# Kernel optimization log

Hardware: AMD Instinct MI355X
Metric: run time of the kernel (lower is better)

The kernel has to match this reference:

```python
import jax, jax.numpy as jnp
import numpy as np

B, L, D, FF = 4, 4096, 1024, 2048
EPS = 1e-5


def _ln(x, g, b):
    m = jnp.mean(x, axis=-1, keepdims=True)
    v = jnp.var(x, axis=-1, keepdims=True)
    return (x - m) / jnp.sqrt(v + EPS) * g + b


def setup_inputs() -> dict:
    key = jax.random.key(0)
    ks = jax.random.split(key, 9)
    x = jax.random.normal(ks[0], (B, L, D), jnp.float32)
    # phazor init: exp(2j*pi*k/D) * |randn| -> split into re/im float params
    mag = jnp.abs(jax.random.normal(ks[1], (D,), jnp.float32))
    ang = 2.0 * jnp.pi * jnp.arange(D, dtype=jnp.float32) / D
    return dict(
        x=x,
        ln_g=jnp.ones((D,), jnp.float32),
        ln_b=jnp.zeros((D,), jnp.float32),
        fc_w=jax.random.normal(ks[2], (D, D), jnp.float32) * 0.02,
        fc_b=jnp.zeros((D,), jnp.float32),
        w1=jax.random.normal(ks[3], (D, FF), jnp.float32) * 0.02,
        b1=jnp.zeros((FF,), jnp.float32),
        w2=jax.random.normal(ks[4], (FF, D), jnp.float32) * 0.02,
        b2=jnp.zeros((D,), jnp.float32),
        ph_re=mag * jnp.cos(ang),
        ph_im=mag * jnp.sin(ang),
        phi_re=jax.random.normal(ks[5], (D,), jnp.float32),
        phi_im=jax.random.normal(ks[6], (D,), jnp.float32),
        lci_re=jax.random.normal(ks[7], (D,), jnp.float32),
        lci_im=jax.random.normal(ks[8], (D,), jnp.float32),
    )


def _spiral_conv(xn, ph_re, ph_im, phi_re, phi_im, lci_re, lci_im):
    ph = ph_re + 1j * ph_im          # phazor parameter [D]
    phi = phi_re + 1j * phi_im       # phazor_init [D]
    lci = lci_re + 1j * lci_im       # last_conv_init [D]
    a = jnp.abs(ph)
    phz = ph / a * jnp.exp(-a)       # unit direction * decaying magnitude, [D]
    t = jnp.arange(L, dtype=jnp.float32)[:, None]
    prog = jnp.exp(t * jnp.log(phz)[None, :])        # phz**t, [L, D]
    filt = prog * phi[None, :]                       # [L, D]
    filt_fft = jnp.fft.fft(filt, n=2 * L, axis=0)    # [2L, D]
    x_fft = jnp.fft.fft(xn.astype(jnp.complex64), n=2 * L, axis=1)  # [B, 2L, D]
    conv = jnp.fft.ifft(filt_fft[None] * x_fft, axis=1)[:, :L]      # [B, L, D]
    # last_conv is detached in the original (first call uses last_conv_init)
    last = jax.lax.stop_gradient(lci)
    conv = conv + last[None, None, :] * prog[None] * phz[None, None, :]
    return conv.real


def reference(x, ln_g, ln_b, fc_w, fc_b, w1, b1, w2, b2,
              ph_re, ph_im, phi_re, phi_im, lci_re, lci_im):
    xn = _ln(x, ln_g, ln_b)
    c = _spiral_conv(xn, ph_re, ph_im, phi_re, phi_im, lci_re, lci_im)
    y = jax.nn.silu(x @ fc_w + fc_b)
    x2 = c * y + x                  # gated conv + residual (dropout=0 -> identity)
    x3 = _ln(x2, ln_g, ln_b)        # same (shared) LayerNorm instance
    h = jax.nn.silu(x3 @ w1 + b1) @ w2 + b2
    return x2 + h
```

## Files before the change

kernel.cpp:

```cpp
#include <hip/hip_runtime.h>
#include <hip/hip_bf16.h>
#include <hip/hip_fp8.h>
#include <cstdint>
#include <cstddef>

#define B_ 4
#define L_ 4096
#define D_ 1024
#define FF_ 2048
#define ROWS (B_ * L_)
#define EPS_ 1e-5f
#define CG 64
#define CC 64

typedef __attribute__((ext_vector_type(8))) __bf16 bf16x8;
typedef __attribute__((ext_vector_type(4))) float f32x4;
typedef __attribute__((ext_vector_type(4))) unsigned short us4;

__device__ __forceinline__ float bf2f(unsigned short u) {
  union { unsigned int i; float f; } v; v.i = ((unsigned int)u) << 16; return v.f;
}
__device__ __forceinline__ unsigned short f2bf(float f) {
  union { float f; unsigned int i; } v; v.f = f;
  unsigned int r = v.i + 0x7fffu + ((v.i >> 16) & 1u);
  return (unsigned short)(r >> 16);
}
__device__ __forceinline__ unsigned char f2fp8(float f) {
  __hip_fp8_e4m3 q(f);
  return *reinterpret_cast<unsigned char*>(&q);
}

__global__ __launch_bounds__(256) void transpose_cast(
    const float* __restrict__ in, unsigned short* __restrict__ out, int K, int N) {
  __shared__ float tb[32][33];
  int n0 = blockIdx.x * 32, k0 = blockIdx.y * 32;
  int tx = threadIdx.x & 31, ty = threadIdx.x >> 5;
#pragma unroll
  for (int i = 0; i < 4; ++i) {
    int k = ty + i * 8;
    tb[k][tx] = in[(size_t)(k0 + k) * N + n0 + tx];
  }
  __syncthreads();
#pragma unroll
  for (int i = 0; i < 4; ++i) {
    int n = ty + i * 8;
    out[(size_t)(n0 + n) * K + k0 + tx] = f2bf(tb[tx][n]);
  }
}

__global__ __launch_bounds__(256) void transpose_cast_fp8(
    const float* __restrict__ in, unsigned char* __restrict__ out, int K, int N,
    float scale) {
  __shared__ float tb[32][33];
  int n0 = blockIdx.x * 32, k0 = blockIdx.y * 32;
  int tx = threadIdx.x & 31, ty = threadIdx.x >> 5;
#pragma unroll
  for (int i = 0; i < 4; ++i) {
    int k = ty + i * 8;
    tb[k][tx] = in[(size_t)(k0 + k) * N + n0 + tx];
  }
  __syncthreads();
#pragma unroll
  for (int i = 0; i < 4; ++i) {
    int n = ty + i * 8;
    out[(size_t)(n0 + n) * K + k0 + tx] = f2fp8(tb[tx][n] * scale);
  }
}

__global__ __launch_bounds__(256) void ln1_kernel(
    const float* __restrict__ x, const float* __restrict__ g, const float* __restrict__ b,
    unsigned short* __restrict__ xn, unsigned short* __restrict__ xb) {
  int row = blockIdx.x;
  int t = threadIdx.x;
  const float4* xr = (const float4*)(x + (size_t)row * D_);
  float4 v = xr[t];
  float s = v.x + v.y + v.z + v.w;
  float sq = v.x * v.x + v.y * v.y + v.z * v.z + v.w * v.w;
#pragma unroll
  for (int off = 32; off > 0; off >>= 1) {
    s += __shfl_down(s, off);
    sq += __shfl_down(sq, off);
  }
  __shared__ float ls[4], lq[4];
  int lane = t & 63, w = t >> 6;
  if (lane == 0) { ls[w] = s; lq[w] = sq; }
  __syncthreads();
  s = ls[0] + ls[1] + ls[2] + ls[3];
  sq = lq[0] + lq[1] + lq[2] + lq[3];
  float mean = s * (1.0f / D_);
  float var = sq * (1.0f / D_) - mean * mean;
  float rstd = rsqrtf(var + EPS_);
  float4 gv = ((const float4*)g)[t];
  float4 bv = ((const float4*)b)[t];
  us4 o, ob;
  o.x = f2bf((v.x - mean) * rstd * gv.x + bv.x);
  o.y = f2bf((v.y - mean) * rstd * gv.y + bv.y);
  o.z = f2bf((v.z - mean) * rstd * gv.z + bv.z);
  o.w = f2bf((v.w - mean) * rstd * gv.w + bv.w);
  ob.x = f2bf(v.x); ob.y = f2bf(v.y); ob.z = f2bf(v.z); ob.w = f2bf(v.w);
  ((us4*)(xn + (size_t)row * D_))[t] = o;
  ((us4*)(xb + (size_t)row * D_))[t] = ob;
}

__global__ __launch_bounds__(256) void conv_pass1(
    const unsigned short* __restrict__ xn, const float* __restrict__ ph_re,
    const float* __restrict__ ph_im, float2* __restrict__ rloc) {
  int d = blockIdx.x * 256 + threadIdx.x;
  int g = blockIdx.y, b = blockIdx.z;
  float re = ph_re[d], im = ph_im[d];
  float a = sqrtf(re * re + im * im);
  float sc = expf(-a) / a;
  float pr = re * sc, pi = im * sc;
  float rr = 0.f, ri = 0.f;
  const unsigned short* xp = xn + ((size_t)(b * L_ + g * CC)) * D_ + d;
#pragma unroll 8
  for (int l = 0; l < CC; ++l) {
    float xv = bf2f(xp[(size_t)l * D_]);
    float nr = pr * rr - pi * ri + xv;
    ri = pr * ri + pi * rr;
    rr = nr;
  }
  rloc[((size_t)(b * CG + g)) * D_ + d] = make_float2(rr, ri);
}

__global__ __launch_bounds__(256) void conv_pass2(
    const float* __restrict__ ph_re, const float* __restrict__ ph_im,
    const float2* __restrict__ rloc, float2* __restrict__ carry) {
  int idx = blockIdx.x * 256 + threadIdx.x;
  int b = idx >> 10, d = idx & (D_ - 1);
  float re = ph_re[d], im = ph_im[d];
  float a = sqrtf(re * re + im * im);
  float th = atan2f(im, re);
  float rho = expf(-a * (float)CC);
  float ang = th * (float)CC;
  float pcr = rho * cosf(ang), pci = rho * sinf(ang);
  float cr = 0.f, ci = 0.f;
  for (int g0 = 0; g0 < CG; g0 += 8) {
    float2 rl[8];
    float2 cw[8];
#pragma unroll
    for (int i = 0; i < 8; ++i)
      rl[i] = rloc[((size_t)(b * CG + g0 + i)) * D_ + d];
#pragma unroll
    for (int i = 0; i < 8; ++i) {
      cw[i] = make_float2(cr, ci);
      float nr = pcr * cr - pci * ci + rl[i].x;
      ci = pcr * ci + pci * cr + rl[i].y;
      cr = nr;
    }
#pragma unroll
    for (int i = 0; i < 8; ++i)
      carry[((size_t)(b * CG + g0 + i)) * D_ + d] = cw[i];
  }
}

__global__ __launch_bounds__(256) void conv_pass3(
    const unsigned short* __restrict__ xn,
    const float* __restrict__ ph_re, const float* __restrict__ ph_im,
    const float* __restrict__ phi_re, const float* __restrict__ phi_im,
    const float* __restrict__ lci_re, const float* __restrict__ lci_im,
    const float2* __restrict__ carry, unsigned short* __restrict__ cout) {
  int d = blockIdx.x * 256 + threadIdx.x;
  int g = blockIdx.y, b = blockIdx.z;
  float re = ph_re[d], im = ph_im[d];
  float a = sqrtf(re * re + im * im);
  float sc = expf(-a) / a;
  float pr = re * sc, pi = im * sc;
  float th = atan2f(im, re);
  int l0 = g * CC;
  float rho = expf(-a * (float)(l0 + 1));
  float ang = th * (float)(l0 + 1);
  float prr = rho * cosf(ang), pri = rho * sinf(ang);
  float fr = phi_re[d], fi = phi_im[d];
  float qr = lci_re[d], qi = lci_im[d];
  float2 cv = carry[((size_t)(b * CG + g)) * D_ + d];
  float rr = cv.x, ri = cv.y;
  const unsigned short* xp = xn + ((size_t)(b * L_ + l0)) * D_ + d;
  unsigned short* cp = cout + ((size_t)(b * L_ + l0)) * D_ + d;
#pragma unroll 4
  for (int l = 0; l < CC; ++l) {
    float xv = bf2f(xp[(size_t)l * D_]);
    float nr = pr * rr - pi * ri + xv;
    ri = pr * ri + pi * rr;
    rr = nr;
    float outv = fr * rr - fi * ri + qr * prr - qi * pri;
    cp[(size_t)l * D_] = f2bf(outv);
    float pn = pr * prr - pi * pri;
    pri = pr * pri + pi * prr;
    prr = pn;
  }
}

__global__ __launch_bounds__(256) void ln2c_kernel(
    const unsigned short* __restrict__ x2, const float* __restrict__ g,
    const float* __restrict__ b, unsigned char* __restrict__ x3) {
  int row = blockIdx.x;
  int t = threadIdx.x;
  size_t base = (size_t)row * D_;
  us4 vb = ((const us4*)(x2 + base))[t];
  float4 v;
  v.x = bf2f(vb.x); v.y = bf2f(vb.y); v.z = bf2f(vb.z); v.w = bf2f(vb.w);
  float s = v.x + v.y + v.z + v.w;
  float sq = v.x * v.x + v.y * v.y + v.z * v.z + v.w * v.w;
#pragma unroll
  for (int off = 32; off > 0; off >>= 1) {
    s += __shfl_down(s, off);
    sq += __shfl_down(sq, off);
  }
  __shared__ float ls[4], lq[4];
  int lane = t & 63, w = t >> 6;
  if (lane == 0) { ls[w] = s; lq[w] = sq; }
  __syncthreads();
  s = ls[0] + ls[1] + ls[2] + ls[3];
  sq = lq[0] + lq[1] + lq[2] + lq[3];
  float mean = s * (1.0f / D_);
  float var = sq * (1.0f / D_) - mean * mean;
  float rstd = rsqrtf(var + EPS_);
  float4 gv = ((const float4*)g)[t];
  float4 bv = ((const float4*)b)[t];
  uchar4 o;
  o.x = f2fp8((v.x - mean) * rstd * gv.x + bv.x);
  o.y = f2fp8((v.y - mean) * rstd * gv.y + bv.y);
  o.z = f2fp8((v.z - mean) * rstd * gv.z + bv.z);
  o.w = f2fp8((v.w - mean) * rstd * gv.w + bv.w);
  ((uchar4*)(x3 + base))[t] = o;
}

__device__ __forceinline__ void gld_lds16(const void* gp, void* lp) {
  __builtin_amdgcn_global_load_lds(
      (const __attribute__((address_space(1))) unsigned int*)gp,
      (__attribute__((address_space(3))) unsigned int*)lp, 16, 0, 0);
}

#define PHASE_SYNC()                                         \
  __builtin_amdgcn_s_barrier();                              \
  asm volatile("s_waitcnt lgkmcnt(0)" ::: "memory");         \
  __builtin_amdgcn_sched_barrier(0);                         \
  __builtin_amdgcn_s_setprio(1);

#define PHASE_END()                                          \
  __builtin_amdgcn_s_setprio(0);

__global__ __launch_bounds__(512) void gemm_bt_gate(
    const unsigned short* __restrict__ A, const unsigned short* __restrict__ Bt,
    const float* __restrict__ bias,
    const unsigned short* __restrict__ gate, const float* __restrict__ xresf,
    unsigned short* __restrict__ Cv, int NB, int GROUP, int N, int K) {
  __shared__ unsigned short As[3][256 * 64];
  __shared__ unsigned short Bs[3][128 * 64];

  int nwg = gridDim.x;
  int xcd = blockIdx.x & 7;
  int lo = blockIdx.x >> 3;
  int q = nwg >> 3;
  int gsz = GROUP * NB;
  int g_ = lo / gsz, r_ = lo % gsz;
  int n_ = r_ / GROUP, ml = r_ - n_ * GROUP;
  int Mx = q / NB;
  int bm0 = (xcd * Mx + g_ * GROUP + ml) * 256;
  int bn0 = n_ * 128;

  int t = threadIdx.x;
  int lane = t & 63, w = t >> 6;
  int wr = w >> 1, wc = w & 1;
  int frr = lane & 15, cl = lane >> 4;
  int fx = frr & 7;
  int rA0 = wr * 64 + frr;
  int rB0 = wc * 64 + frr;
  int ko0 = (cl ^ fx) * 8;
  int ko1 = ((4 + cl) ^ fx) * 8;

  int nt = K >> 6;

  int tr = t >> 3;
  int jx = (t & 7) ^ (tr & 7);
  const unsigned short* pA = A + (size_t)(bm0 + tr) * K + jx * 8;
  const unsigned short* pB = Bt + (size_t)(bn0 + tr) * K + jx * 8;

  auto stA = [&](int kt2, int slot, int c) {
    gld_lds16(pA + (size_t)kt2 * 64 + (size_t)c * 64 * K, &As[slot][c * 4096 + t * 8]);
  };
  auto stB = [&](int kt2, int slot, int c) {
    gld_lds16(pB + (size_t)kt2 * 64 + (size_t)c * 64 * K, &Bs[slot][c * 4096 + t * 8]);
  };

  f32x4 acc[4][4] = {};

  stA(0, 0, 0); stA(0, 0, 1); stA(0, 0, 2); stA(0, 0, 3); stB(0, 0, 0); stB(0, 0, 1);
  stA(1, 1, 0); stA(1, 1, 1); stA(1, 1, 2); stA(1, 1, 3); stB(1, 1, 0); stB(1, 1, 1);
  asm volatile("s_waitcnt vmcnt(6)" ::: "memory");
  __builtin_amdgcn_s_barrier();

  int s = 0;
  for (int kt = 0; kt < nt; ++kt) {
    const unsigned short* as = As[s];
    const unsigned short* bs = Bs[s];
    int s2 = s + 2; if (s2 >= 3) s2 -= 3;
    bool p2 = kt + 2 < nt;

    bf16x8 a0[4], b0[4];
#pragma unroll
    for (int m = 0; m < 4; ++m) a0[m] = *(const bf16x8*)&as[(rA0 + m * 16) * 64 + ko0];
#pragma unroll
    for (int n = 0; n < 4; ++n) b0[n] = *(const bf16x8*)&bs[(rB0 + n * 16) * 64 + ko0];
    if (p2) { stA(kt + 2, s2, 0); stA(kt + 2, s2, 1); stB(kt + 2, s2, 0); }
    PHASE_SYNC();
#pragma unroll
    for (int m = 0; m < 4; ++m)
#pragma unroll
      for (int n = 0; n < 4; ++n)
        acc[m][n] = __builtin_amdgcn_mfma_f32_16x16x32_bf16(a0[m], b0[n], acc[m][n], 0, 0, 0);
    PHASE_END();
    __builtin_amdgcn_s_barrier();

    bf16x8 a1[4], b1[4];
#pragma unroll
    for (int m = 0; m < 4; ++m) a1[m] = *(const bf16x8*)&as[(rA0 + m * 16) * 64 + ko1];
#pragma unroll
    for (int n = 0; n < 4; ++n) b1[n] = *(const bf16x8*)&bs[(rB0 + n * 16) * 64 + ko1];
    if (p2) { stA(kt + 2, s2, 2); stA(kt + 2, s2, 3); stB(kt + 2, s2, 1); }
    PHASE_SYNC();
#pragma unroll
    for (int m = 0; m < 4; ++m)
#pragma unroll
      for (int n = 0; n < 4; ++n)
        acc[m][n] = __builtin_amdgcn_mfma_f32_16x16x32_bf16(a1[m], b1[n], acc[m][n], 0, 0, 0);
    PHASE_END();
    if (p2) { asm volatile("s_waitcnt vmcnt(6)" ::: "memory"); }
    else    { asm volatile("s_waitcnt vmcnt(0)" ::: "memory"); }
    __builtin_amdgcn_s_barrier();
    s += 1; if (s == 3) s = 0;
  }

#pragma unroll
  for (int m = 0; m < 4; ++m) {
#pragma unroll
    for (int n = 0; n < 4; ++n) {
#pragma unroll
      for (int r = 0; r < 4; ++r) {
        int row = bm0 + wr * 64 + m * 16 + cl * 4 + r;
        int col = bn0 + wc * 64 + n * 16 + frr;
        size_t o = (size_t)row * N + col;
        float v = acc[m][n][r] + bias[col];
        v = v / (1.0f + __expf(-v));
        v = bf2f(gate[o]) * v + xresf[o];
        Cv[o] = f2bf(v);
      }
    }
  }
}

template <int SILU, int RESBF, int OUT_FP8>
__global__ __launch_bounds__(512, 4) void gemm_f8(
    const unsigned char* __restrict__ A, const unsigned char* __restrict__ Bt,
    const float* __restrict__ bias, const unsigned short* __restrict__ resb,
    float oscale, void* __restrict__ Cv, int NB, int GROUP, int N, int K) {
  __shared__ unsigned char As[3][256 * 64];
  __shared__ unsigned char Bs[3][128 * 64];

  int nwg = gridDim.x;
  int xcd = blockIdx.x & 7;
  int lo = blockIdx.x >> 3;
  int q = nwg >> 3;
  int gsz = GROUP * NB;
  int g_ = lo / gsz, r_ = lo % gsz;
  int n_ = r_ / GROUP, ml = r_ - n_ * GROUP;
  int Mx = q / NB;
  int bm0 = (xcd * Mx + g_ * GROUP + ml) * 256;
  int bn0 = n_ * 128;

  int t = threadIdx.x;
  int lane = t & 63, w = t >> 6;
  int wr = w >> 1, wc = w & 1;
  int frr = lane & 15, cl = lane >> 4;
  int sw = (frr >> 1) & 3;
  int rA0 = wr * 64 + frr;
  int rB0 = wc * 64 + frr;
  int ko0 = ((((cl >> 1) ^ sw) << 4) | ((cl & 1) << 3));
  int ko1 = (((((cl >> 1) + 2) ^ sw) << 4) | ((cl & 1) << 3));

  int nt = K >> 6;

  int tr = t >> 2;
  int jc = (t & 3) ^ ((tr >> 1) & 3);
  const unsigned char* pA = A + (size_t)(bm0 + tr) * K + jc * 16;
  const unsigned char* pB = Bt + (size_t)(bn0 + tr) * K + jc * 16;

  auto stA = [&](int kt2, int slot, int c) {
    gld_lds16(pA + (size_t)kt2 * 64 + (size_t)c * 128 * K, &As[slot][c * 8192 + t * 16]);
  };
  auto stB = [&](int kt2, int slot) {
    gld_lds16(pB + (size_t)kt2 * 64, &Bs[slot][t * 16]);
  };

  f32x4 acc[4][4] = {};

  stA(0, 0, 0); stA(0, 0, 1); stB(0, 0);
  stA(1, 1, 0); stA(1, 1, 1); stB(1, 1);
  asm volatile("s_waitcnt vmcnt(3)" ::: "memory");
  __builtin_amdgcn_s_barrier();

  int s = 0;
  for (int kt = 0; kt < nt; ++kt) {
    const unsigned char* as = As[s];
    const unsigned char* bs = Bs[s];
    int s2 = s + 2; if (s2 >= 3) s2 -= 3;
    bool p2 = kt + 2 < nt;

    long a0[4], b0[4], a1[4], b1[4];
#pragma unroll
    for (int m = 0; m < 4; ++m) a0[m] = *(const long*)&as[(rA0 + m * 16) * 64 + ko0];
#pragma unroll
    for (int n = 0; n < 4; ++n) b0[n] = *(const long*)&bs[(rB0 + n * 16) * 64 + ko0];
#pragma unroll
    for (int m = 0; m < 4; ++m) a1[m] = *(const long*)&as[(rA0 + m * 16) * 64 + ko1];
#pragma unroll
    for (int n = 0; n < 4; ++n) b1[n] = *(const long*)&bs[(rB0 + n * 16) * 64 + ko1];
    if (p2) { stA(kt + 2, s2, 0); stA(kt + 2, s2, 1); stB(kt + 2, s2); }

    asm volatile("s_waitcnt lgkmcnt(0)" ::: "memory");
    __builtin_amdgcn_sched_barrier(0);
    __builtin_amdgcn_s_setprio(1);
#pragma unroll
    for (int m = 0; m < 4; ++m)
#pragma unroll
      for (int n = 0; n < 4; ++n)
        acc[m][n] = __builtin_amdgcn_mfma_f32_16x16x32_fp8_fp8(a0[m], b0[n], acc[m][n], 0, 0, 0);
#pragma unroll
    for (int m = 0; m < 4; ++m)
#pragma unroll
      for (int n = 0; n < 4; ++n)
        acc[m][n] = __builtin_amdgcn_mfma_f32_16x16x32_fp8_fp8(a1[m], b1[n], acc[m][n], 0, 0, 0);
    __builtin_amdgcn_s_setprio(0);

    if (p2) { asm volatile("s_waitcnt vmcnt(3)" ::: "memory"); }
    else    { asm volatile("s_waitcnt vmcnt(0)" ::: "memory"); }
    __builtin_amdgcn_s_barrier();
    s += 1; if (s == 3) s = 0;
  }

#pragma unroll
  for (int m = 0; m < 4; ++m) {
#pragma unroll
    for (int n = 0; n < 4; ++n) {
#pragma unroll
      for (int r = 0; r < 4; ++r) {
        int row = bm0 + wr * 64 + m * 16 + cl * 4 + r;
        int col = bn0 + wc * 64 + n * 16 + frr;
        size_t o = (size_t)row * N + col;
        float v = acc[m][n][r] * oscale + bias[col];
        if (SILU) v = v / (1.0f + __expf(-v));
        if (RESBF) v += bf2f(resb[o]);
        if (OUT_FP8)
          ((unsigned char*)Cv)[o] = f2fp8(v);
        else
          ((float*)Cv)[o] = v;
      }
    }
  }
}

extern "C" void kernel_launch(void* const* d_in, const int* in_sizes, int n_in,
                              void* d_out, int out_size, void* d_ws, size_t ws_size,
                              hipStream_t stream) {
  const float* x      = (const float*)d_in[0];
  const float* ln_g   = (const float*)d_in[1];
  const float* ln_b   = (const float*)d_in[2];
  const float* fc_w   = (const float*)d_in[3];
  const float* fc_b   = (const float*)d_in[4];
  const float* w1     = (const float*)d_in[5];
  const float* b1     = (const float*)d_in[6];
  const float* w2     = (const float*)d_in[7];
  const float* b2     = (const float*)d_in[8];
  const float* ph_re  = (const float*)d_in[9];
  const float* ph_im  = (const float*)d_in[10];
  const float* phi_re = (const float*)d_in[11];
  const float* phi_im = (const float*)d_in[12];
  const float* lci_re = (const float*)d_in[13];
  const float* lci_im = (const float*)d_in[14];
  float* out = (float*)d_out;

  char* ws = (char*)d_ws;
  const size_t SZ_BF = (size_t)ROWS * D_ * 2;
  const size_t SZ_F8 = (size_t)ROWS * D_;
  unsigned short* xn_x2 = (unsigned short*)(ws);
  unsigned short* cbuf  = (unsigned short*)(ws + SZ_BF);
  unsigned short* xb    = (unsigned short*)(ws + 2 * SZ_BF);
  unsigned char*  x3f8  = (unsigned char*)(ws + 3 * SZ_BF);
  unsigned char*  h1f8  = (unsigned char*)(ws + 3 * SZ_BF + SZ_F8);
  char* wp = ws + 3 * SZ_BF + SZ_F8 + (size_t)ROWS * FF_;
  unsigned short* fc_wt = (unsigned short*)(wp);
  unsigned char*  w1t8  = (unsigned char*)(wp + (size_t)D_ * D_ * 2);
  unsigned char*  w2t8  = (unsigned char*)(wp + (size_t)D_ * D_ * 2 + (size_t)D_ * FF_);
  float2* rloc  = (float2*)(wp + (size_t)D_ * D_ * 2 + 2 * (size_t)D_ * FF_);
  float2* carry = rloc + (size_t)B_ * CG * D_;

  transpose_cast<<<dim3(D_ / 32, D_ / 32), 256, 0, stream>>>(fc_w, fc_wt, D_, D_);
  transpose_cast_fp8<<<dim3(FF_ / 32, D_ / 32), 256, 0, stream>>>(w1, w1t8, D_, FF_, 32.0f);
  transpose_cast_fp8<<<dim3(D_ / 32, FF_ / 32), 256, 0, stream>>>(w2, w2t8, FF_, D_, 32.0f);

  ln1_kernel<<<ROWS, 256, 0, stream>>>(x, ln_g, ln_b, xn_x2, xb);

  conv_pass1<<<dim3(D_ / 256, CG, B_), 256, 0, stream>>>(xn_x2, ph_re, ph_im, rloc);
  conv_pass2<<<dim3((B_ * D_) / 256), 256, 0, stream>>>(ph_re, ph_im, rloc, carry);
  conv_pass3<<<dim3(D_ / 256, CG, B_), 256, 0, stream>>>(xn_x2, ph_re, ph_im, phi_re, phi_im,
                                                         lci_re, lci_im, carry, cbuf);

  gemm_bt_gate<<<(ROWS / 256) * (D_ / 128), 512, 0, stream>>>(
      xb, fc_wt, fc_b, cbuf, x, xn_x2, D_ / 128, 4, D_, D_);

  ln2c_kernel<<<ROWS, 256, 0, stream>>>(xn_x2, ln_g, ln_b, x3f8);

  gemm_f8<1, 0, 1><<<(ROWS / 256) * (FF_ / 128), 512, 0, stream>>>(
      x3f8, w1t8, b1, nullptr, 1.0f / 32.0f, h1f8, FF_ / 128, 4, FF_, D_);

  gemm_f8<0, 1, 0><<<(ROWS / 256) * (D_ / 128), 512, 0, stream>>>(
      h1f8, w2t8, b2, xn_x2, 1.0f / 32.0f, out, D_ / 128, 2, D_, FF_);
}
```

Baseline: 269.5 us.

## Permute FP8 operand layout for 128-bit LDS reads; single-phase bf16 gate GEMM loop

The FP8 operands (transposed weights, LN2 output, FF1 output) are now written in a permuted order within each 64-byte K chunk. This lets the FP8 GEMM fetch both k-halves with a single 16-byte LDS read per fragment instead of two 8-byte reads. Separately, the bf16 gate GEMM drops its two-phase barrier-split loop: it loads all fragments up front, issues all prefetches together, and runs both MFMA halves under one priority raise. The risk is that every producer and consumer must agree on the permutation, and the bf16 loop loses the intra-tile barrier overlap while holding more fragment registers live.

```diff
diff --git a/kernel.cpp b/kernel.cpp
--- a/kernel.cpp
+++ b/kernel.cpp
@@ -16,6 +16,7 @@
 typedef __attribute__((ext_vector_type(8))) __bf16 bf16x8;
 typedef __attribute__((ext_vector_type(4))) float f32x4;
 typedef __attribute__((ext_vector_type(4))) unsigned short us4;
+typedef __attribute__((ext_vector_type(2))) long l2;
 
 __device__ __forceinline__ float bf2f(unsigned short u) {
   union { unsigned int i; float f; } v; v.i = ((unsigned int)u) << 16; return v.f;
@@ -28,6 +29,9 @@
 __device__ __forceinline__ unsigned char f2fp8(float f) {
   __hip_fp8_e4m3 q(f);
   return *reinterpret_cast<unsigned char*>(&q);
+}
+__device__ __forceinline__ int ph64(int e) {
+  return (((e >> 3) & 3) << 4) | (((e >> 5) & 1) << 3) | (e & 7);
 }
 
 __global__ __launch_bounds__(256) void transpose_cast(
@@ -63,7 +67,9 @@
 #pragma unroll
   for (int i = 0; i < 4; ++i) {
     int n = ty + i * 8;
-    out[(size_t)(n0 + n) * K + k0 + tx] = f2fp8(tb[tx][n] * scale);
+    int k = k0 + tx;
+    size_t idx = (size_t)(n0 + n) * K + (k & ~63) + ph64(k & 63);
+    out[idx] = f2fp8(tb[tx][n] * scale);
   }
 }
 
@@ -223,7 +229,9 @@
   o.y = f2fp8((v.y - mean) * rstd * gv.y + bv.y);
   o.z = f2fp8((v.z - mean) * rstd * gv.z + bv.z);
   o.w = f2fp8((v.w - mean) * rstd * gv.w + bv.w);
-  ((uchar4*)(x3 + base))[t] = o;
+  int d = t * 4;
+  size_t idx = base + (size_t)((d & ~63) + ph64(d & 63));
+  *((uchar4*)(x3 + idx)) = o;
 }
 
 __device__ __forceinline__ void gld_lds16(const void* gp, void* lp) {
@@ -231,15 +239,6 @@
       (const __attribute__((address_space(1))) unsigned int*)gp,
       (__attribute__((address_space(3))) unsigned int*)lp, 16, 0, 0);
 }
-
-#define PHASE_SYNC()                                         \
-  __builtin_amdgcn_s_barrier();                              \
-  asm volatile("s_waitcnt lgkmcnt(0)" ::: "memory");         \
-  __builtin_amdgcn_sched_barrier(0);                         \
-  __builtin_amdgcn_s_setprio(1);
-
-#define PHASE_END()                                          \
-  __builtin_amdgcn_s_setprio(0);
 
 __global__ __launch_bounds__(512) void gemm_bt_gate(
     const unsigned short* __restrict__ A, const unsigned short* __restrict__ Bt,
@@ -298,34 +297,35 @@
     int s2 = s + 2; if (s2 >= 3) s2 -= 3;
     bool p2 = kt + 2 < nt;
 
-    bf16x8 a0[4], b0[4];
+    bf16x8 a0[4], b0[4], a1[4], b1[4];
 #pragma unroll
     for (int m = 0; m < 4; ++m) a0[m] = *(const bf16x8*)&as[(rA0 + m * 16) * 64 + ko0];
 #pragma unroll
     for (int n = 0; n < 4; ++n) b0[n] = *(const bf16x8*)&bs[(rB0 + n * 16) * 64 + ko0];
-    if (p2) { stA(kt + 2, s2, 0); stA(kt + 2, s2, 1); stB(kt + 2, s2, 0); }
-    PHASE_SYNC();
+#pragma unroll
+    for (int m = 0; m < 4; ++m) a1[m] = *(const bf16x8*)&as[(rA0 + m * 16) * 64 + ko1];
+#pragma unroll
+    for (int n = 0; n < 4; ++n) b1[n] = *(const bf16x8*)&bs[(rB0 + n * 16) * 64 + ko1];
+    if (p2) {
+      stA(kt + 2, s2, 0); stA(kt + 2, s2, 1); stA(kt + 2, s2, 2); stA(kt + 2, s2, 3);
+      stB(kt + 2, s2, 0); stB(kt + 2, s2, 1);
+    }
+
+    asm volatile("s_waitcnt lgkmcnt(0)" ::: "memory");
+    __builtin_amdgcn_sched_barrier(0);
+    __builtin_amdgcn_s_setprio(1);
 #pragma unroll
     for (int m = 0; m < 4; ++m)
 #pragma unroll
       for (int n = 0; n < 4; ++n)
         acc[m][n] = __builtin_amdgcn_mfma_f32_16x16x32_bf16(a0[m], b0[n], acc[m][n], 0, 0, 0);
-    PHASE_END();
-    __builtin_amdgcn_s_barrier();
-
-    bf16x8 a1[4], b1[4];
-#pragma unroll
-    for (int m = 0; m < 4; ++m) a1[m] = *(const bf16x8*)&as[(rA0 + m * 16) * 64 + ko1];
-#pragma unroll
-    for (int n = 0; n < 4; ++n) b1[n] = *(const bf16x8*)&bs[(rB0 + n * 16) * 64 + ko1];
-    if (p2) { stA(kt + 2, s2, 2); stA(kt + 2, s2, 3); stB(kt + 2, s2, 1); }
-    PHASE_SYNC();
 #pragma unroll
     for (int m = 0; m < 4; ++m)
 #pragma unroll
       for (int n = 0; n < 4; ++n)
         acc[m][n] = __builtin_amdgcn_mfma_f32_16x16x32_bf16(a1[m], b1[n], acc[m][n], 0, 0, 0);
-    PHASE_END();
+    __builtin_amdgcn_s_setprio(0);
+
     if (p2) { asm volatile("s_waitcnt vmcnt(6)" ::: "memory"); }
     else    { asm volatile("s_waitcnt vmcnt(0)" ::: "memory"); }
     __builtin_amdgcn_s_barrier();
@@ -376,8 +376,7 @@
   int sw = (frr >> 1) & 3;
   int rA0 = wr * 64 + frr;
   int rB0 = wc * 64 + frr;
-  int ko0 = ((((cl >> 1) ^ sw) << 4) | ((cl & 1) << 3));
-  int ko1 = (((((cl >> 1) + 2) ^ sw) << 4) | ((cl & 1) << 3));
+  int ko = (cl ^ sw) * 16;
 
   int nt = K >> 6;
 
@@ -407,15 +406,11 @@
     int s2 = s + 2; if (s2 >= 3) s2 -= 3;
     bool p2 = kt + 2 < nt;
 
-    long a0[4], b0[4], a1[4], b1[4];
-#pragma unroll
-    for (int m = 0; m < 4; ++m) a0[m] = *(const long*)&as[(rA0 + m * 16) * 64 + ko0];
-#pragma unroll
-    for (int n = 0; n < 4; ++n) b0[n] = *(const long*)&bs[(rB0 + n * 16) * 64 + ko0];
-#pragma unroll
-    for (int m = 0; m < 4; ++m) a1[m] = *(const long*)&as[(rA0 + m * 16) * 64 + ko1];
-#pragma unroll
-    for (int n = 0; n < 4; ++n) b1[n] = *(const long*)&bs[(rB0 + n * 16) * 64 + ko1];
+    l2 av[4], bv[4];
+#pragma unroll
+    for (int m = 0; m < 4; ++m) av[m] = *(const l2*)&as[(rA0 + m * 16) * 64 + ko];
+#pragma unroll
+    for (int n = 0; n < 4; ++n) bv[n] = *(const l2*)&bs[(rB0 + n * 16) * 64 + ko];
     if (p2) { stA(kt + 2, s2, 0); stA(kt + 2, s2, 1); stB(kt + 2, s2); }
 
     asm volatile("s_waitcnt lgkmcnt(0)" ::: "memory");
@@ -425,12 +420,12 @@
     for (int m = 0; m < 4; ++m)
 #pragma unroll
       for (int n = 0; n < 4; ++n)
-        acc[m][n] = __builtin_amdgcn_mfma_f32_16x16x32_fp8_fp8(a0[m], b0[n], acc[m][n], 0, 0, 0);
+        acc[m][n] = __builtin_amdgcn_mfma_f32_16x16x32_fp8_fp8(av[m].x, bv[n].x, acc[m][n], 0, 0, 0);
 #pragma unroll
     for (int m = 0; m < 4; ++m)
 #pragma unroll
       for (int n = 0; n < 4; ++n)
-        acc[m][n] = __builtin_amdgcn_mfma_f32_16x16x32_fp8_fp8(a1[m], b1[n], acc[m][n], 0, 0, 0);
+        acc[m][n] = __builtin_amdgcn_mfma_f32_16x16x32_fp8_fp8(av[m].y, bv[n].y, acc[m][n], 0, 0, 0);
     __builtin_amdgcn_s_setprio(0);
 
     if (p2) { asm volatile("s_waitcnt vmcnt(3)" ::: "memory"); }
@@ -451,10 +446,13 @@
         float v = acc[m][n][r] * oscale + bias[col];
         if (SILU) v = v / (1.0f + __expf(-v));
         if (RESBF) v += bf2f(resb[o]);
-        if (OUT_FP8)
-          ((unsigned char*)Cv)[o] = f2fp8(v);
-        else
+        if (OUT_FP8) {
+          int e = n * 16 + frr;
+          size_t op = (size_t)row * N + bn0 + wc * 64 + ph64(e);
+          ((unsigned char*)Cv)[op] = f2fp8(v);
+        } else {
           ((float*)Cv)[o] = v;
+        }
       }
     }
   }
```

Measured after the change: 259.6 us. -3.7%, faster.
